# Kernel optimization log

Hardware: AMD Instinct MI355X
Metric: run time of the kernel (lower is better)

Reference implementation:

```python
import jax, jax.numpy as jnp
import numpy as np

B, N, K = 4, 1024, 512
HEADS, DH = 8, 64
HID = 2048
KAPPA = 1.0      # kappa_beta
ALPHA = 1e-3     # ffn_alpha (prior weight)
LAM = 1.0        # ffn_lambda_belief
NITER = 2        # ffn_n_iterations
EPS = 1e-8


def _ln(x, g, b):
    m = jnp.mean(x, axis=-1, keepdims=True)
    v = jnp.var(x, axis=-1, keepdims=True)
    return (x - m) * jax.lax.rsqrt(v + 1e-5) * g + b


def _transport(x, phi, G):
    # truncated exp(phi . G) applied to x without materializing (B,N,K,K)
    def Ax(y):
        return jnp.einsum('bng,gkl,bnl->bnk', phi, G, y)
    a1 = Ax(x)
    return x + a1 + 0.5 * Ax(a1)


def setup_inputs() -> dict:
    key = jax.random.key(0)
    ks = jax.random.split(key, 16)
    mu_q = jax.random.normal(ks[0], (B, N, K), dtype=jnp.float32)
    sigma_q = jax.random.uniform(ks[1], (B, N, K), minval=0.5, maxval=1.5, dtype=jnp.float32)
    phi = 0.1 * jax.random.normal(ks[2], (B, N, 3), dtype=jnp.float32)
    A = jax.random.normal(ks[3], (3, K, K), dtype=jnp.float32)
    generators = 0.05 * (A - jnp.transpose(A, (0, 2, 1)))  # antisymmetric Lie generators
    mask = jnp.broadcast_to(jnp.tril(jnp.ones((N, N), dtype=bool)), (B, N, N))  # causal
    mu_prior = jax.random.normal(ks[4], (B, N, K), dtype=jnp.float32)
    s = 0.02
    Wq = s * jax.random.normal(ks[5], (K, K), dtype=jnp.float32)
    Wk = s * jax.random.normal(ks[6], (K, K), dtype=jnp.float32)
    Wv = s * jax.random.normal(ks[7], (K, K), dtype=jnp.float32)
    Wo = s * jax.random.normal(ks[8], (K, K), dtype=jnp.float32)
    g1 = jnp.ones((K,), jnp.float32); be1 = jnp.zeros((K,), jnp.float32)
    g2 = jnp.ones((K,), jnp.float32); be2 = jnp.zeros((K,), jnp.float32)
    W1 = s * jax.random.normal(ks[9], (K, HID), dtype=jnp.float32)
    bh1 = jnp.zeros((HID,), jnp.float32)
    W2 = s * jax.random.normal(ks[10], (HID, K), dtype=jnp.float32)
    bh2 = jnp.zeros((K,), jnp.float32)
    lr = jnp.array(0.1, jnp.float32)  # learnable VFE step size
    return {'mu_q': mu_q, 'sigma_q': sigma_q, 'phi': phi, 'generators': generators,
            'mask': mask, 'mu_prior': mu_prior, 'Wq': Wq, 'Wk': Wk, 'Wv': Wv, 'Wo': Wo,
            'g1': g1, 'be1': be1, 'g2': g2, 'be2': be2,
            'W1': W1, 'bh1': bh1, 'W2': W2, 'bh2': bh2, 'lr': lr}


def reference(mu_q, sigma_q, phi, generators, mask, mu_prior,
              Wq, Wk, Wv, Wo, g1, be1, g2, be2, W1, bh1, W2, bh2, lr):
    # ---- attention sublayer ----
    mu_n = _ln(mu_q, g1, be1)
    mu_g = _transport(mu_n, phi, generators)  # transport to common frame

    def heads(x):  # (B,N,K) -> (B,H,N,Dh)
        return x.reshape(B, N, HEADS, DH).transpose(0, 2, 1, 3)

    q = heads(mu_g @ Wq)
    k = heads(mu_g @ Wk)
    v = heads(mu_g @ Wv)
    # diagonal covariance propagated through linear maps: var_out = sigma @ W^2
    sq = heads(sigma_q @ (Wq * Wq)) + EPS
    sk = heads(sigma_q @ (Wk * Wk)) + EPS

    inv = 1.0 / sq
    # KL(N(k_j,sk_j) || N(q_i,sq_i)) for diagonal Gaussians, decomposed into matmuls
    tr = jnp.einsum('bhid,bhjd->bhij', inv, sk)
    quad = (jnp.sum(q * q * inv, axis=-1)[..., None]
            - 2.0 * jnp.einsum('bhid,bhjd->bhij', q * inv, k)
            + jnp.einsum('bhid,bhjd->bhij', inv, k * k))
    logdet = (jnp.sum(jnp.log(sq), axis=-1)[..., None]
              - jnp.sum(jnp.log(sk), axis=-1)[:, :, None, :])
    kl = 0.5 * (tr + quad - DH + logdet)  # (B,H,N,N)

    scores = jnp.where(mask[:, None, :, :], -kl / KAPPA, -1e9)
    beta = jax.nn.softmax(scores, axis=-1)

    out = jnp.einsum('bhij,bhjd->bhid', beta, v)
    out = out.transpose(0, 2, 1, 3).reshape(B, N, K)
    mu_attn = _transport(out @ Wo, -phi, generators)  # back-transport to local frames
    mu_res = mu_q + mu_attn  # residual (dropout is identity in eval)

    # ---- VFE_dynamic FFN sublayer ----
    mu_n2 = _ln(mu_res, g2, be2)
    beta_m = jnp.mean(beta, axis=1)  # (B,N,N) attention-belief coupling
    h = mu_n2
    for _ in range(NITER):
        drive = jax.nn.gelu(h @ W1 + bh1) @ W2 + bh2
        grad = ALPHA * (h - mu_prior) + LAM * (h - jnp.einsum('bij,bjk->bik', beta_m, h))
        h = h + lr * (drive - grad)
    mu_out = mu_res + (h - mu_n2)

    return (mu_out, sigma_q, phi)
```

## Files before the change

kernel.cpp:

```cpp
#include <hip/hip_runtime.h>
#include <math.h>

#define BB 4
#define NN 1024
#define KK 512
#define HH 8
#define DHh 64
#define HIDd 2048
#define BN (BB*NN)

typedef unsigned short u16;
typedef __attribute__((ext_vector_type(8))) short bf16x8;
typedef __attribute__((ext_vector_type(4))) float f32x4;

__device__ __forceinline__ float gelu_tanh(float x){
    float u = 0.7978845608028654f*(x + 0.044715f*x*x*x);
    u = fminf(fmaxf(u, -15.f), 15.f);
    float t = __expf(2.f*u);
    return x*t/(t+1.f);
}
__device__ __forceinline__ u16 f2bf(float x){
    unsigned int u = __float_as_uint(x);
    unsigned int r = (u + 0x7fffu + ((u>>16)&1u)) >> 16;
    return (u16)r;
}
__device__ __forceinline__ float bf2f(u16 b){
    return __uint_as_float(((unsigned int)b)<<16);
}
__device__ __forceinline__ void gload16(const void* g, void* l){
    __builtin_amdgcn_global_load_lds((__attribute__((address_space(1))) void*)g,
                                     (__attribute__((address_space(3))) void*)l, 16, 0, 0);
}
__device__ __forceinline__ void wsplit(u16* hi, u16* lo, size_t o, float v){
    u16 h = f2bf(v);
    hi[o] = h;
    if (lo) lo[o] = f2bf(v - bf2f(h));
}

__global__ __launch_bounds__(256) void split_t_k(
    const float* __restrict__ src, u16* __restrict__ hi, u16* __restrict__ lo,
    int Kc, int Nc, long sS, long sD, int square)
{
    __shared__ float t[32][33];
    const int n0 = blockIdx.x*32, k0 = blockIdx.y*32, bz = blockIdx.z;
    const float* S = src + (long)bz*sS;
    const int tx = threadIdx.x & 31, ty = threadIdx.x >> 5;
    for (int r = ty; r < 32; r += 8){
        float v = S[(long)(k0+r)*Nc + n0+tx];
        if (square) v *= v;
        t[r][tx] = v;
    }
    __syncthreads();
    for (int r = ty; r < 32; r += 8){
        float v = t[tx][r];
        long o = (long)bz*sD + (long)(n0+r)*Kc + k0 + tx;
        wsplit(hi, lo, o, v);
    }
}

__global__ __launch_bounds__(256) void wmega_k(
    const float* __restrict__ Wq, const float* __restrict__ Wk,
    const float* __restrict__ Wv, const float* __restrict__ Wo,
    const float* __restrict__ W1, const float* __restrict__ W2,
    const float* __restrict__ gen,
    u16* __restrict__ WQKVh, u16* __restrict__ WQKVl, u16* __restrict__ WoTh,
    u16* __restrict__ WSQKh, u16* __restrict__ WSQKl,
    u16* __restrict__ W1Th, u16* __restrict__ W2Th, u16* __restrict__ GFh)
{
    const int z = blockIdx.z;
    const int tid = threadIdx.x;
    if (z == 8){
        if (blockIdx.x >= 48) return;
        const int c0 = blockIdx.x*32, k0 = blockIdx.y*32;
        const int tx = tid&31, ty = tid>>5;
        const int g = c0/KK, l0 = c0%KK;
        for (int r=ty; r<32; r+=8)
            GFh[(size_t)(k0+r)*(3*KK) + c0+tx] =
                f2bf(gen[(size_t)g*KK*KK + (size_t)(k0+r)*KK + l0+tx]);
        return;
    }
    __shared__ float t[32][33];
    const float* src; u16* hi; u16* lo=0; int sq=0;
    int n0, k0, Kc, Nc;
    const size_t KK2 = (size_t)KK*KK;
    if (z < 6){
        if (blockIdx.x >= 16) return;
        n0 = blockIdx.x*32; k0 = blockIdx.y*32; Kc=KK; Nc=KK;
        if      (z==0){ src=Wq; hi=WQKVh;       lo=WQKVl; }
        else if (z==1){ src=Wk; hi=WQKVh+KK2;   lo=WQKVl+KK2; }
        else if (z==2){ src=Wv; hi=WQKVh+2*KK2; lo=WQKVl+2*KK2; }
        else if (z==3){ src=Wo; hi=WoTh; }
        else if (z==4){ src=Wq; hi=WSQKh;       lo=WSQKl; sq=1; }
        else          { src=Wk; hi=WSQKh+KK2;   lo=WSQKl+KK2; sq=1; }
    } else if (z == 6){
        src=W1; hi=W1Th; Kc=KK; Nc=HIDd;
        n0 = blockIdx.x*32; k0 = blockIdx.y*32;
    } else {
        src=W2; hi=W2Th; Kc=HIDd; Nc=KK;
        n0 = blockIdx.y*32; k0 = blockIdx.x*32;
    }
    const int tx=tid&31, ty=tid>>5;
    for (int r=ty;r<32;r+=8){
        float v = src[(long)(k0+r)*Nc + n0+tx];
        if (sq) v*=v;
        t[r][tx]=v;
    }
    __syncthreads();
    for (int r=ty;r<32;r+=8){
        float v = t[tx][r];
        long o = (long)(n0+r)*Kc + k0+tx;
        wsplit(hi, lo, o, v);
    }
}

__global__ __launch_bounds__(256) void gemm_mfma_k(
    const u16* __restrict__ Ah, const u16* __restrict__ Bh,
    float* __restrict__ C, u16* __restrict__ Chi, u16* __restrict__ Clo,
    int M, int Kc, int Nc, int lda,
    long sA, long sB, long sC, const float* __restrict__ bias, int act,
    int swz)
{
    __shared__ u16 shA[2][128*32], shB[2][128*32];
    int bx = blockIdx.x, by = blockIdx.y;
    if (swz){
        int lin = bx + gridDim.x*by;
        int within = lin & 31, st = lin >> 5;
        int stm = gridDim.x >> 3;
        bx = (st % stm)*8 + (within & 7);
        by = (st / stm)*4 + (within >> 3);
    }
    const int m0 = bx*128, n0 = by*128;
    const int bz = blockIdx.z;
    const u16* gAh = Ah + (long)bz*sA;
    const u16* gBh = Bh + (long)bz*sB;
    const int tid = threadIdx.x;
    const int wave = tid >> 6, lane = tid & 63;
    const int quad = lane >> 4, r16 = lane & 15;
    const int wm = (wave>>1)*64, wn = (wave&1)*64;

    f32x4 acc[4][4];
    #pragma unroll
    for (int i=0;i<4;i++)
        #pragma unroll
        for (int j=0;j<4;j++) acc[i][j] = (f32x4){0.f,0.f,0.f,0.f};

    auto stage = [&](int sel, int k0){
        #pragma unroll
        for (int half=0; half<2; ++half){
            int c = half*256 + tid;
            int row = c >> 2;
            int kg = ((c & 3) ^ ((row >> 1) & 3))*8;
            gload16(gAh + (long)(m0+row)*lda + k0 + kg, &shA[sel][c*8]);
            gload16(gBh + (long)(n0+row)*Kc  + k0 + kg, &shB[sel][c*8]);
        }
    };

    const int nsteps = Kc >> 5;
    stage(0, 0);
    __syncthreads();
    int cur = 0;
    const int swr = (quad ^ ((r16 >> 1) & 3))*8;
    for (int t = 0; t < nsteps; ++t){
        if (t+1 < nsteps) stage(cur^1, (t+1)<<5);
        bf16x8 afh[4], bfh[4];
        #pragma unroll
        for (int i=0;i<4;i++){
            afh[i] = *(const bf16x8*)&shA[cur][(wm+i*16+r16)*32 + swr];
            bfh[i] = *(const bf16x8*)&shB[cur][(wn+i*16+r16)*32 + swr];
        }
        #pragma unroll
        for (int i=0;i<4;i++)
            #pragma unroll
            for (int j=0;j<4;j++)
                acc[i][j] = __builtin_amdgcn_mfma_f32_16x16x32_bf16(afh[i], bfh[j], acc[i][j], 0,0,0);
        __syncthreads();
        cur ^= 1;
    }
    #pragma unroll
    for (int i=0;i<4;i++){
        #pragma unroll
        for (int j=0;j<4;j++){
            int gc = n0 + wn + j*16 + r16;
            if (gc >= Nc) continue;
            float bv = bias ? bias[gc] : 0.f;
            #pragma unroll
            for (int r=0;r<4;r++){
                long gr = m0 + wm + i*16 + quad*4 + r;
                float v = acc[i][j][r] + bv;
                if (act) v = gelu_tanh(v);
                long o = (long)bz*sC + gr*Nc + gc;
                if (C) C[o] = v;
                if (Chi){ u16 t = f2bf(v); Chi[o] = t; if (Clo) Clo[o] = f2bf(v - bf2f(t)); }
            }
        }
    }
}

__global__ __launch_bounds__(256) void gemm_v3_k(
    const u16* __restrict__ Ah, const u16* __restrict__ Al,
    const u16* __restrict__ Bh, const u16* __restrict__ Bl,
    float* __restrict__ C,
    int M, int Kc, int Nc, int lda,
    long sA, long sB, long sC, int cskip)
{
    __shared__ u16 shA[2][128*32], shB[2][128*32];
    const int m0 = blockIdx.x*128, n0 = blockIdx.y*128;
    if (cskip == 1 && n0 > m0 + 127) return;
    const int bz = blockIdx.z;
    const u16* gAh = Ah + (long)bz*sA;
    const u16* gAl = Al + (long)bz*sA;
    const u16* gBh = Bh + (long)bz*sB;
    const u16* gBl = Bl + (long)bz*sB;
    const int tid = threadIdx.x;
    const int wave = tid >> 6, lane = tid & 63;
    const int quad = lane >> 4, r16 = lane & 15;
    const int wm = (wave>>1)*64, wn = (wave&1)*64;

    f32x4 acc[4][4];
    #pragma unroll
    for (int i=0;i<4;i++)
        #pragma unroll
        for (int j=0;j<4;j++) acc[i][j] = (f32x4){0.f,0.f,0.f,0.f};

    const int segsteps = Kc >> 5;
    const int nsteps = 3*segsteps;
    auto stage = [&](int sel, int t){
        int seg = (t >= segsteps) + (t >= 2*segsteps);
        int k0 = (t - seg*segsteps) << 5;
        const u16* a = (seg==1) ? gAl : gAh;
        const u16* b = (seg==2) ? gBl : gBh;
        #pragma unroll
        for (int half=0; half<2; ++half){
            int c = half*256 + tid;
            int row = c >> 2;
            int kg = ((c & 3) ^ ((row >> 1) & 3))*8;
            gload16(a + (long)(m0+row)*lda + k0 + kg, &shA[sel][c*8]);
            gload16(b + (long)(n0+row)*Kc  + k0 + kg, &shB[sel][c*8]);
        }
    };

    stage(0, 0);
    __syncthreads();
    int cur = 0;
    const int swr = (quad ^ ((r16 >> 1) & 3))*8;
    for (int t = 0; t < nsteps; ++t){
        if (t+1 < nsteps) stage(cur^1, t+1);
        bf16x8 afh[4], bfh[4];
        #pragma unroll
        for (int i=0;i<4;i++){
            afh[i] = *(const bf16x8*)&shA[cur][(wm+i*16+r16)*32 + swr];
            bfh[i] = *(const bf16x8*)&shB[cur][(wn+i*16+r16)*32 + swr];
        }
        #pragma unroll
        for (int i=0;i<4;i++)
            #pragma unroll
            for (int j=0;j<4;j++)
                acc[i][j] = __builtin_amdgcn_mfma_f32_16x16x32_bf16(afh[i], bfh[j], acc[i][j], 0,0,0);
        __syncthreads();
        cur ^= 1;
    }
    #pragma unroll
    for (int i=0;i<4;i++){
        #pragma unroll
        for (int j=0;j<4;j++){
            int gc = n0 + wn + j*16 + r16;
            if (gc >= Nc) continue;
            #pragma unroll
            for (int r=0;r<4;r++){
                long gr = m0 + wm + i*16 + quad*4 + r;
                long o = (long)bz*sC + gr*Nc + gc;
                C[o] = acc[i][j][r];
            }
        }
    }
}

__global__ __launch_bounds__(256) void tgemm_k(
    const u16* __restrict__ Ahh,
    const u16* __restrict__ GFh,
    const float* __restrict__ phi, float esign,
    float* __restrict__ C, u16* __restrict__ Chi, u16* __restrict__ Clo,
    const float* __restrict__ t_x, const float* __restrict__ t_a1,
    const float* __restrict__ t_res)
{
    __shared__ u16 shA[2][64*64], shB[2][64*64];
    const int m0 = blockIdx.x*64, n0 = blockIdx.y*64;
    const int tid = threadIdx.x;
    const int wave = tid >> 6, lane = tid & 63;
    const int quad = lane >> 4, r16 = lane & 15;
    const int wr = wave*16;

    float ph[3][4];
    #pragma unroll
    for (int sgi=0; sgi<3; ++sgi)
        #pragma unroll
        for (int r=0; r<4; ++r)
            ph[sgi][r] = esign*phi[(size_t)(m0+wr+quad*4+r)*3 + sgi];

    f32x4 acc[4], tot[4];
    #pragma unroll
    for (int j=0;j<4;j++){ acc[j] = (f32x4){0.f,0.f,0.f,0.f}; tot[j] = acc[j]; }

    auto stage = [&](int sel, int t){
        int seg = t >> 3, k0 = (t & 7) << 6;
        #pragma unroll
        for (int rep=0; rep<2; ++rep){
            int c = rep*256 + tid;
            int row = c >> 3;
            int kg = ((c & 7) ^ (row & 7))*8;
            gload16(Ahh + (long)(m0+row)*KK + k0 + kg, &shA[sel][c*8]);
            gload16(GFh + (long)(n0+row)*(3*KK) + seg*KK + k0 + kg, &shB[sel][c*8]);
        }
    };

    stage(0, 0);
    __syncthreads();
    int cur = 0;
    for (int t = 0; t < 24; ++t){
        if (t+1 < 24) stage(cur^1, t+1);
        #pragma unroll
        for (int kk=0; kk<2; ++kk){
            const int s = (((kk<<2)+quad) ^ (r16 & 7))*8;
            bf16x8 af = *(const bf16x8*)&shA[cur][(wr+r16)*64 + s];
            #pragma unroll
            for (int j=0;j<4;j++){
                bf16x8 bh = *(const bf16x8*)&shB[cur][(j*16+r16)*64 + s];
                acc[j] = __builtin_amdgcn_mfma_f32_16x16x32_bf16(af, bh, acc[j], 0,0,0);
            }
        }
        if ((t & 7) == 7){
            int sgi = t >> 3;
            #pragma unroll
            for (int j=0;j<4;j++){
                #pragma unroll
                for (int r=0;r<4;r++) tot[j][r] += ph[sgi][r]*acc[j][r];
                acc[j] = (f32x4){0.f,0.f,0.f,0.f};
            }
        }
        __syncthreads();
        cur ^= 1;
    }
    #pragma unroll
    for (int j=0;j<4;j++){
        int gc = n0 + j*16 + r16;
        #pragma unroll
        for (int r=0;r<4;r++){
            long gr = m0 + wr + quad*4 + r;
            float v = tot[j][r];
            long o = gr*(long)KK + gc;
            if (t_x){
                v = t_x[o] + t_a1[o] + 0.5f*v;
                if (t_res) v += t_res[o];
            }
            if (C) C[o] = v;
            if (Chi){ u16 t2 = f2bf(v); Chi[o] = t2; if (Clo) Clo[o] = f2bf(v - bf2f(t2)); }
        }
    }
}

__global__ __launch_bounds__(256) void gemm64_k(
    const u16* __restrict__ Ah, const u16* __restrict__ Bh,
    float* __restrict__ C, u16* __restrict__ Chi, u16* __restrict__ Clo,
    int M, int Kc, int Nc, int lda,
    long sA, long sB, long sC, const float* __restrict__ bias, int act,
    int ktrim, int swz,
    const float* __restrict__ f_hin, const float* __restrict__ f_bmh,
    const float* __restrict__ f_mup, const float* __restrict__ f_lr,
    u16* __restrict__ f_hh, float* __restrict__ f_hout,
    const float* __restrict__ f_mrb, const float* __restrict__ f_mn2,
    float* __restrict__ f_out, int fmode)
{
    __shared__ u16 shA[2][64*64], shB[2][64*64];
    int bx = blockIdx.x, by = blockIdx.y;
    if (swz){
        int lin = bx + gridDim.x*by;
        int within = lin & 31, st = lin >> 5;
        int stm = gridDim.x >> 3;
        bx = (st % stm)*8 + (within & 7);
        by = (st / stm)*4 + (within >> 3);
    }
    const int m0 = bx*64, n0 = by*64;
    const int bz = blockIdx.z;
    const u16* gA = Ah + (long)bz*sA;
    const u16* gB = Bh + (long)bz*sB;
    const int tid = threadIdx.x;
    const int wave = tid >> 6, lane = tid & 63;
    const int quad = lane >> 4, r16 = lane & 15;
    const int wr = wave*16;
    const int kend = ktrim ? min(Kc, m0 + 64) : Kc;
    const int nsteps = kend >> 6;

    f32x4 acc[4];
    #pragma unroll
    for (int j=0;j<4;j++) acc[j] = (f32x4){0.f,0.f,0.f,0.f};

    auto stage = [&](int sel, int k0){
        #pragma unroll
        for (int rep=0; rep<2; ++rep){
            int c = rep*256 + tid;
            int row = c >> 3;
            int kg = ((c & 7) ^ (row & 7))*8;
            gload16(gA + (long)(m0+row)*lda + k0 + kg, &shA[sel][c*8]);
            gload16(gB + (long)(n0+row)*Kc + k0 + kg, &shB[sel][c*8]);
        }
    };

    stage(0, 0);
    __syncthreads();
    int cur = 0;
    for (int t = 0; t < nsteps; ++t){
        if (t+1 < nsteps) stage(cur^1, (t+1)<<6);
        #pragma unroll
        for (int kk=0; kk<2; ++kk){
            const int s = (((kk<<2)+quad) ^ (r16 & 7))*8;
            bf16x8 af = *(const bf16x8*)&shA[cur][(wr+r16)*64 + s];
            #pragma unroll
            for (int j=0;j<4;j++){
                bf16x8 bh = *(const bf16x8*)&shB[cur][(j*16+r16)*64 + s];
                acc[j] = __builtin_amdgcn_mfma_f32_16x16x32_bf16(af, bh, acc[j], 0,0,0);
            }
        }
        __syncthreads();
        cur ^= 1;
    }
    float lrv = 0.f;
    if (fmode) lrv = *f_lr;
    #pragma unroll
    for (int j=0;j<4;j++){
        int gc = n0 + j*16 + r16;
        float bv = bias ? bias[gc] : 0.f;
        #pragma unroll
        for (int r=0;r<4;r++){
            long gr = m0 + wr + quad*4 + r;
            float v = acc[j][r] + bv;
            if (act) v = gelu_tanh(v);
            long o = (long)bz*sC + gr*Nc + gc;
            if (fmode){
                float hv = f_hin[o];
                float val = hv + lrv*(v - (1e-3f*(hv - f_mup[o]) + (hv - f_bmh[o])));
                if (fmode == 1){ f_hout[o] = val; f_hh[o] = f2bf(val); }
                else           { f_out[o] = f_mrb[o] + val - f_mn2[o]; }
            } else {
                if (C) C[o] = v;
                if (Chi){ u16 t = f2bf(v); Chi[o] = t; if (Clo) Clo[o] = f2bf(v - bf2f(t)); }
            }
        }
    }
}

__global__ __launch_bounds__(256) void ln_k(
    const float* __restrict__ x, const float* __restrict__ g,
    const float* __restrict__ be, float* __restrict__ y,
    u16* __restrict__ yh16,
    const float* __restrict__ sg, u16* __restrict__ sgh, u16* __restrict__ sgl,
    float* __restrict__ osig, const float* __restrict__ phi, float* __restrict__ ophi)
{
    __shared__ float sh[8];
    const int r = blockIdx.x, tid = threadIdx.x;
    const float* xr = x + (long)r*KK;
    float2 v = *(const float2*)(xr + tid*2);
    float s = v.x+v.y, s2 = v.x*v.x+v.y*v.y;
    #pragma unroll
    for (int o=32;o>0;o>>=1){ s += __shfl_down(s,o); s2 += __shfl_down(s2,o); }
    if ((tid&63)==0){ sh[tid>>6]=s; sh[4+(tid>>6)]=s2; }
    __syncthreads();
    s  = sh[0]+sh[1]+sh[2]+sh[3];
    s2 = sh[4]+sh[5]+sh[6]+sh[7];
    const float mean = s*(1.f/KK);
    const float var  = s2*(1.f/KK) - mean*mean;
    const float rs = rsqrtf(var + 1e-5f);
    float2 gg = *(const float2*)(g + tid*2);
    float2 bb = *(const float2*)(be + tid*2);
    float ox = (v.x-mean)*rs*gg.x + bb.x;
    float oy = (v.y-mean)*rs*gg.y + bb.y;
    long o = (long)r*KK + tid*2;
    *(float2*)(y + o) = make_float2(ox, oy);
    if (yh16){ yh16[o] = f2bf(ox); yh16[o+1] = f2bf(oy); }
    if (sgh){
        float2 sv = *(const float2*)(sg + o);
        wsplit(sgh, sgl, o,   sv.x);
        wsplit(sgh, sgl, o+1, sv.y);
        if (osig) *(float2*)(osig + o) = sv;
    }
    if (ophi && tid < 3) ophi[(size_t)r*3 + tid] = phi[(size_t)r*3 + tid];
}

__global__ __launch_bounds__(512) void prepvt_k(
    const float* __restrict__ QKV, const float* __restrict__ SQSK,
    u16* __restrict__ CFh, u16* __restrict__ CFl,
    u16* __restrict__ KSh, u16* __restrict__ KSl, float* __restrict__ dvec,
    u16* __restrict__ VTh)
{
    __shared__ float t[64][65];
    const int bx = blockIdx.x;
    const int tid = threadIdx.x;
    if (bx < BN){
        const int bn = bx;
        const int b = bn / NN, n = bn % NN;
        const int h = tid >> 6, d = tid & 63;
        float q  = QKV[(size_t)bn*1536 + h*DHh + d];
        float k  = QKV[(size_t)bn*1536 + KK + h*DHh + d];
        float sq = SQSK[(size_t)bn*1024 + h*DHh + d] + 1e-8f;
        float sk = SQSK[(size_t)bn*1024 + KK + h*DHh + d] + 1e-8f;
        float inv = 1.f/sq;
        float nqi = -2.f*q*inv;
        float skk = sk + k*k;
        const size_t base = ((size_t)(h*BB + b)*NN + n)*128;
        wsplit(CFh, CFl, base+d,    inv);
        wsplit(CFh, CFl, base+64+d, nqi);
        wsplit(KSh, KSl, base+d,    skk);
        wsplit(KSh, KSl, base+64+d, k);
        float dv = __logf(sk);
        #pragma unroll
        for (int o=32;o>0;o>>=1) dv += __shfl_down(dv,o);
        if (d==0) dvec[((size_t)h*BB + b)*NN + n] = dv;
        return;
    }
    const int idx = bx - BN;
    const int n0 = (idx & 15)*64;
    const int h = (idx>>4)&7;
    const int b = idx>>7;
    const int c4 = (tid & 15) * 4;
    const int r0 = tid >> 4;
    for (int rr = r0; rr < 64; rr += 32){
        float4 v = *(const float4*)(QKV + (size_t)(b*NN + n0 + rr)*1536 + 1024 + h*DHh + c4);
        t[c4+0][rr] = v.x; t[c4+1][rr] = v.y; t[c4+2][rr] = v.z; t[c4+3][rr] = v.w;
    }
    __syncthreads();
    for (int dd = r0; dd < 64; dd += 32){
        size_t base = ((size_t)(h*BB + b)*64 + dd)*NN + n0 + c4;
        #pragma unroll
        for (int q=0;q<4;q++) VTh[base+q] = f2bf(t[dd][c4+q]);
    }
}

__global__ __launch_bounds__(256) void softmax_all_k(
    float* __restrict__ S, const float* __restrict__ dvec, u16* __restrict__ BMh)
{
    __shared__ float s_sc[NN];
    __shared__ float s_bm[NN];
    __shared__ float s_red[4];
    const int tid = threadIdx.x;
    const int b = blockIdx.x / NN, i = blockIdx.x % NN;
    const int L = i + 1;
    const int JEND = ((i >> 6) + 1) << 6;
    for (int j=tid;j<JEND;j+=256) s_bm[j]=0.f;
    for (int h=0; h<8; ++h){
        const int z = h*BB + b;
        float* row = S + ((long)z*NN + i)*NN;
        const float* dp = dvec + (size_t)z*NN;
        float lm = -3.0e38f;
        for (int j=tid;j<L;j+=256){
            float sc = -0.5f*row[j] + 0.5f*dp[j];
            s_sc[j] = sc;
            lm = fmaxf(lm, sc);
        }
        #pragma unroll
        for (int o=32;o>0;o>>=1) lm = fmaxf(lm, __shfl_xor(lm, o));
        __syncthreads();
        if ((tid&63)==0) s_red[tid>>6] = lm;
        __syncthreads();
        const float mx = fmaxf(fmaxf(s_red[0],s_red[1]), fmaxf(s_red[2],s_red[3]));
        float ps = 0.f;
        for (int j=tid;j<L;j+=256){
            float e = __expf(s_sc[j]-mx);
            s_sc[j] = e;
            ps += e;
        }
        #pragma unroll
        for (int o=32;o>0;o>>=1) ps += __shfl_xor(ps, o);
        __syncthreads();
        if ((tid&63)==0) s_red[tid>>6] = ps;
        __syncthreads();
        const float isum = 1.f/(s_red[0]+s_red[1]+s_red[2]+s_red[3]);
        u16* brow = (u16*)row;
        for (int j=tid;j<JEND;j+=256){
            if (j < L){
                float w = s_sc[j]*isum;
                brow[j] = f2bf(w);
                s_bm[j] += 0.125f*w;
            } else {
                brow[j] = 0;
            }
        }
        __syncthreads();
    }
    const long bmrow = ((long)b*NN + i)*NN;
    for (int j=tid;j<JEND;j+=256) BMh[bmrow+j] = f2bf(s_bm[j]);
}

__global__ __launch_bounds__(256) void pv_k(
    const u16* __restrict__ Sbeta,
    const u16* __restrict__ VTh,
    u16* __restrict__ xh)
{
    __shared__ u16 shA[2][64*64], shB[2][64*64];
    const int m0 = blockIdx.x*64;
    const int z = blockIdx.y;
    const int b = z & 3, head = z >> 2;
    const int tid = threadIdx.x;
    const int wave = tid>>6, lane = tid&63;
    const int quad = lane>>4, r16 = lane&15;
    f32x4 acc[4];
    #pragma unroll
    for (int j=0;j<4;j++) acc[j]=(f32x4){0.f,0.f,0.f,0.f};
    const int nsteps = (m0 >> 6) + 1;

    auto stage = [&](int sel, int j0){
        #pragma unroll
        for (int rep=0; rep<2; ++rep){
            int c = rep*256 + tid;
            int row = c >> 3;
            int k8 = ((c & 7) ^ (row & 7))*8;
            gload16(Sbeta + ((size_t)(z*NN + m0 + row))*(2*NN) + j0 + k8, &shA[sel][c*8]);
            gload16(VTh + ((size_t)(z*64 + row))*NN + j0 + k8, &shB[sel][c*8]);
        }
    };

    stage(0, 0);
    __syncthreads();
    int cur = 0;
    for (int t = 0; t < nsteps; ++t){
        if (t+1 < nsteps) stage(cur^1, (t+1)<<6);
        #pragma unroll
        for (int kk=0; kk<2; ++kk){
            const int s = (((kk<<2)+quad) ^ (r16 & 7))*8;
            bf16x8 af = *(const bf16x8*)&shA[cur][(wave*16 + r16)*64 + s];
            #pragma unroll
            for (int nj=0; nj<4; ++nj){
                bf16x8 bh = *(const bf16x8*)&shB[cur][(nj*16 + r16)*64 + s];
                acc[nj] = __builtin_amdgcn_mfma_f32_16x16x32_bf16(af, bh, acc[nj], 0,0,0);
            }
        }
        __syncthreads();
        cur ^= 1;
    }
    #pragma unroll
    for (int nj=0;nj<4;nj++){
        #pragma unroll
        for (int r=0;r<4;r++){
            int i = m0 + wave*16 + quad*4 + r;
            int d = nj*16 + r16;
            size_t o = ((size_t)(b*NN)+i)*KK + head*64 + d;
            xh[o] = f2bf(acc[nj][r]);
        }
    }
}

extern "C" void kernel_launch(void* const* d_in, const int* in_sizes, int n_in,
                              void* d_out, int out_size, void* d_ws, size_t ws_size,
                              hipStream_t stream) {
    const float* mu_q    = (const float*)d_in[0];
    const float* sigma_q = (const float*)d_in[1];
    const float* phi     = (const float*)d_in[2];
    const float* gen     = (const float*)d_in[3];
    const float* mu_prior= (const float*)d_in[5];
    const float* Wq = (const float*)d_in[6];
    const float* Wk = (const float*)d_in[7];
    const float* Wv = (const float*)d_in[8];
    const float* Wo = (const float*)d_in[9];
    const float* g1 = (const float*)d_in[10];
    const float* be1= (const float*)d_in[11];
    const float* g2 = (const float*)d_in[12];
    const float* be2= (const float*)d_in[13];
    const float* W1 = (const float*)d_in[14];
    const float* bh1= (const float*)d_in[15];
    const float* W2 = (const float*)d_in[16];
    const float* bh2= (const float*)d_in[17];
    const float* lr = (const float*)d_in[18];
    float* out = (float*)d_out;

    float* w = (float*)d_ws;
    size_t off = 0;
    auto alloc = [&](size_t n){ float* p = w + off; off += (n+3)&~(size_t)3; return p; };
    auto ualloc = [&](size_t n){ return (u16*)alloc((n+1)/2); };

    float* Xb   = alloc((size_t)BN*KK);
    float* A1b  = alloc((size_t)BN*KK);
    float* A2b  = alloc((size_t)BN*KK);
    float* QKVb = alloc((size_t)BN*3*KK);
    float* SQSKb= alloc((size_t)BN*2*KK);
    float* REG  = alloc((size_t)16*NN*NN);
    float* Sbig = Xb;
    u16*  SGh   = (u16*)REG;
    u16*  SGl   = SGh + (size_t)BN*KK;
    u16*  Xh    = SGl + (size_t)BN*KK;
    u16*  A1h   = Xh  + (size_t)BN*KK;
    u16*  WOh   = A1h + (size_t)BN*KK;
    u16*  ZH    = (u16*)REG;
    float* Db_  = alloc((size_t)HH*BB*NN);
    u16* AH  = ualloc((size_t)BN*HIDd); u16* AL  = ualloc((size_t)BN*HIDd);
    u16* CFh = AH;
    u16* CFl = AH + (size_t)HH*BB*NN*128;
    u16* KSh = AL;
    u16* KSl = AL + (size_t)HH*BB*NN*128;
    u16* VTh = ualloc((size_t)HH*BB*64*NN);
    u16* GFh = ualloc((size_t)3*KK*KK);
    u16* WQKVh= ualloc((size_t)3*KK*KK); u16* WQKVl= ualloc((size_t)3*KK*KK);
    u16* WSQKh= ualloc((size_t)2*KK*KK); u16* WSQKl= ualloc((size_t)2*KK*KK);
    u16* WoTh= ualloc((size_t)KK*KK);
    u16* W1Th= ualloc((size_t)KK*HIDd);
    u16* W2Th= ualloc((size_t)KK*HIDd);
    u16* BMh = ualloc((size_t)BB*NN*NN);
    u16* HTh = ualloc((size_t)BB*KK*NN);
    float* WOb = QKVb;
    float* Hb  = QKVb + (size_t)BN*KK;
    float* MRb = QKVb + 2*(size_t)BN*KK;
    float* MN2b= Xb;
    (void)A2b;

    {
        dim3 gw(64, 16, 9);
        wmega_k<<<gw, 256, 0, stream>>>(Wq, Wk, Wv, Wo, W1, W2, gen,
                                        WQKVh, WQKVl, WoTh, WSQKh, WSQKl,
                                        W1Th, W2Th, GFh);
    }

    ln_k<<<BN, 256, 0, stream>>>(mu_q, g1, be1, Xb, Xh, sigma_q, SGh, SGl,
                                 out + (size_t)BN*KK, phi, out + 2*(size_t)BN*KK);
    {
        dim3 tg(BN/64, KK/64, 1);
        tgemm_k<<<tg, 256, 0, stream>>>(Xh, GFh, phi, 1.f, A1b, A1h, 0, 0, 0, 0);
        tgemm_k<<<tg, 256, 0, stream>>>(A1h, GFh, phi, 1.f, 0, AH, AL, Xb, A1b, 0);
    }

    {
        dim3 gq(BN/128, (3*KK)/128, 1);
        gemm_v3_k<<<gq, 256, 0, stream>>>(AH, AL, WQKVh, WQKVl, QKVb,
            BN, KK, 3*KK, KK, 0, 0, 0, 0);
        dim3 gs(BN/128, (2*KK)/128, 1);
        gemm_v3_k<<<gs, 256, 0, stream>>>(SGh, SGl, WSQKh, WSQKl, SQSKb,
            BN, KK, 2*KK, KK, 0, 0, 0, 0);
    }
    prepvt_k<<<BN + 512, 512, 0, stream>>>(QKVb, SQSKb, CFh, CFl, KSh, KSl, Db_, VTh);

    {
        dim3 sg(NN/128, NN/128, 32);
        gemm_v3_k<<<sg, 256, 0, stream>>>(CFh, CFl, KSh, KSl, Sbig,
            NN, 128, NN, 128, (long)NN*128, (long)NN*128, (long)NN*NN, 1);
        softmax_all_k<<<BB*NN, 256, 0, stream>>>(Sbig, Db_, BMh);
        dim3 pg(NN/64, 32, 1);
        pv_k<<<pg, 256, 0, stream>>>((const u16*)Sbig, VTh, AH);
    }

    {
        dim3 wg(BN/64, KK/64, 1);
        gemm64_k<<<wg, 256, 0, stream>>>(AH, WoTh, WOb, WOh, 0,
            BN, KK, KK, KK, 0,0,0, nullptr, 0, 0, 0,
            0,0,0,0,0,0,0,0,0,0);
        dim3 tg(BN/64, KK/64, 1);
        tgemm_k<<<tg, 256, 0, stream>>>(WOh, GFh, phi, -1.f, A1b, A1h, 0, 0, 0, 0);
        tgemm_k<<<tg, 256, 0, stream>>>(A1h, GFh, phi, -1.f, MRb, 0, 0, WOb, A1b, mu_q);
    }
    ln_k<<<BN, 256, 0, stream>>>(MRb, g2, be2, MN2b, AH, 0, 0, 0, 0, 0, 0);

    for (int it=0; it<2; ++it){
        const float* hin = (it==0) ? MN2b : Hb;
        {
            dim3 tg(KK/32, NN/32, BB);
            split_t_k<<<tg, 256, 0, stream>>>(hin, HTh, 0, NN, KK,
                                              (long)NN*KK, (long)KK*NN, 0);
        }
        {
            dim3 bg(NN/64, KK/64, BB);
            gemm64_k<<<bg, 256, 0, stream>>>(BMh, HTh, A1b, 0,0,
                                             NN, NN, KK, NN,
                                             (long)NN*NN, (long)KK*NN, (long)NN*KK,
                                             nullptr, 0, 1, 0,
                                             0,0,0,0,0,0,0,0,0,0);
        }
        {
            dim3 wg1(BN/128, HIDd/128, 1);
            gemm_mfma_k<<<wg1, 256, 0, stream>>>(AH, W1Th, 0, ZH, 0,
                BN, KK, HIDd, KK, 0, 0, 0, bh1, 1, 1);
        }
        {
            dim3 wg(BN/64, KK/64, 1);
            gemm64_k<<<wg, 256, 0, stream>>>(ZH, W2Th, 0,0,0,
                                             BN, HIDd, KK, HIDd, 0,0,0, bh2, 0, 0, 1,
                                             hin, A1b, mu_prior, lr, AH, Hb, MRb, MN2b, out,
                                             (it==0) ? 1 : 2);
        }
    }

    (void)in_sizes; (void)n_in; (void)out_size; (void)ws_size;
}
```

Measured before the change: 605.7 us.

## Register-resident softmax with float4 loads, prefetch of next head, fewer barriers

The per-row softmax over all 8 heads now keeps scores in registers, four contiguous elements per thread, instead of staging them in shared memory. Loads are vectorised float4 and the next head's row is prefetched while the current head is processed. Double-buffered reduction slots cut the barriers per head from five to two, and the head-mean accumulator moves from shared memory to registers. It assumes each row fits in 256*4 = 1024 elements, which holds for N=1024.

```diff
diff --git a/kernel.cpp b/kernel.cpp
--- a/kernel.cpp
+++ b/kernel.cpp
@@ -537,56 +537,72 @@
 __global__ __launch_bounds__(256) void softmax_all_k(
     float* __restrict__ S, const float* __restrict__ dvec, u16* __restrict__ BMh)
 {
-    __shared__ float s_sc[NN];
-    __shared__ float s_bm[NN];
-    __shared__ float s_red[4];
+    __shared__ float s_redA[2][4], s_redB[2][4];
     const int tid = threadIdx.x;
-    const int b = blockIdx.x / NN, i = blockIdx.x % NN;
+    const int b = blockIdx.x >> 10, i = blockIdx.x & (NN-1);
     const int L = i + 1;
     const int JEND = ((i >> 6) + 1) << 6;
-    for (int j=tid;j<JEND;j+=256) s_bm[j]=0.f;
-    for (int h=0; h<8; ++h){
+    const int j4 = tid*4;
+    const bool act = (j4 < JEND);
+    const int wv = tid >> 6;
+    const bool lane0 = ((tid & 63) == 0);
+
+    float bm[4] = {0.f,0.f,0.f,0.f};
+    float4 rv = make_float4(0,0,0,0), dpv = make_float4(0,0,0,0);
+    if (act){
+        rv  = *(const float4*)(S + ((long)(0*BB + b)*NN + i)*NN + j4);
+        dpv = *(const float4*)(dvec + (size_t)(0*BB + b)*NN + j4);
+    }
+    for (int h = 0; h < 8; ++h){
         const int z = h*BB + b;
-        float* row = S + ((long)z*NN + i)*NN;
-        const float* dp = dvec + (size_t)z*NN;
-        float lm = -3.0e38f;
-        for (int j=tid;j<L;j+=256){
-            float sc = -0.5f*row[j] + 0.5f*dp[j];
-            s_sc[j] = sc;
-            lm = fmaxf(lm, sc);
-        }
+        float4 rvn = make_float4(0,0,0,0), dpn = make_float4(0,0,0,0);
+        if (h < 7 && act){
+            const int zn = (h+1)*BB + b;
+            rvn = *(const float4*)(S + ((long)zn*NN + i)*NN + j4);
+            dpn = *(const float4*)(dvec + (size_t)zn*NN + j4);
+        }
+        float sc[4];
+        const float* rp = (const float*)&rv;
+        const float* dp = (const float*)&dpv;
+        #pragma unroll
+        for (int e=0;e<4;e++){
+            float s = -0.5f*rp[e] + 0.5f*dp[e];
+            sc[e] = (act && (j4 + e < L)) ? s : -3.0e38f;
+        }
+        float lm = fmaxf(fmaxf(sc[0],sc[1]), fmaxf(sc[2],sc[3]));
         #pragma unroll
         for (int o=32;o>0;o>>=1) lm = fmaxf(lm, __shfl_xor(lm, o));
+        if (lane0) s_redA[h&1][wv] = lm;
         __syncthreads();
-        if ((tid&63)==0) s_red[tid>>6] = lm;
+        const float mx = fmaxf(fmaxf(s_redA[h&1][0],s_redA[h&1][1]),
+                               fmaxf(s_redA[h&1][2],s_redA[h&1][3]));
+        float w4[4], ps = 0.f;
+        #pragma unroll
+        for (int e=0;e<4;e++){
+            float e1 = (act && (j4 + e < L)) ? __expf(sc[e]-mx) : 0.f;
+            w4[e] = e1; ps += e1;
+        }
+        #pragma unroll
+        for (int o=32;o>0;o>>=1) ps += __shfl_xor(ps, o);
+        if (lane0) s_redB[h&1][wv] = ps;
         __syncthreads();
-        const float mx = fmaxf(fmaxf(s_red[0],s_red[1]), fmaxf(s_red[2],s_red[3]));
-        float ps = 0.f;
-        for (int j=tid;j<L;j+=256){
-            float e = __expf(s_sc[j]-mx);
-            s_sc[j] = e;
-            ps += e;
-        }
-        #pragma unroll
-        for (int o=32;o>0;o>>=1) ps += __shfl_xor(ps, o);
-        __syncthreads();
-        if ((tid&63)==0) s_red[tid>>6] = ps;
-        __syncthreads();
-        const float isum = 1.f/(s_red[0]+s_red[1]+s_red[2]+s_red[3]);
-        u16* brow = (u16*)row;
-        for (int j=tid;j<JEND;j+=256){
-            if (j < L){
-                float w = s_sc[j]*isum;
-                brow[j] = f2bf(w);
-                s_bm[j] += 0.125f*w;
-            } else {
-                brow[j] = 0;
-            }
-        }
-        __syncthreads();
-    }
-    const long bmrow = ((long)b*NN + i)*NN;
-    for (int j=tid;j<JEND;j+=256) BMh[bmrow+j] = f2bf(s_bm[j]);
+        const float isum = 1.f/(s_redB[h&1][0]+s_redB[h&1][1]+s_redB[h&1][2]+s_redB[h&1][3]);
+        if (act){
+            u16* brow = (u16*)(S + ((long)z*NN + i)*NN);
+            ushort4 st;
+            float w0=w4[0]*isum, w1=w4[1]*isum, w2=w4[2]*isum, w3=w4[3]*isum;
+            bm[0]+=0.125f*w0; bm[1]+=0.125f*w1; bm[2]+=0.125f*w2; bm[3]+=0.125f*w3;
+            st.x=f2bf(w0); st.y=f2bf(w1); st.z=f2bf(w2); st.w=f2bf(w3);
+            *(ushort4*)(brow + j4) = st;
+        }
+        rv = rvn; dpv = dpn;
+    }
+    if (act){
+        const long bmrow = ((long)b*NN + i)*NN;
+        ushort4 st;
+        st.x=f2bf(bm[0]); st.y=f2bf(bm[1]); st.z=f2bf(bm[2]); st.w=f2bf(bm[3]);
+        *(ushort4*)(BMh + bmrow + j4) = st;
+    }
 }
 
 __global__ __launch_bounds__(256) void pv_k(
```

After: 585.9 us. 3.3% less time.
